# Kernel optimization log

Measured on AMD Instinct MI355X. Metric: run time of the kernel, lower is better.

## Reference

```python
import jax, jax.numpy as jnp
import numpy as np


def _pairwise_dist(x):
    # Euclidean (p=2) pairwise distances via Gram identity; avoids the
    # [N, N, D] broadcasted difference tensor the torch code materializes.
    sq = jnp.sum(x * x, axis=1)                      # [N]
    d2 = sq[:, None] + sq[None, :] - 2.0 * (x @ x.T)  # [N, N]
    return jnp.sqrt(jnp.clip(d2, 0.0))


def _persistence_pairs(dist_np):
    """0-dim persistent homology pairs = MST edges via Kruskal union-find,
    processed in order of increasing edge weight (matches the repo's
    PersistentHomologyCalculation). Returns [N-1, 2] int64 index pairs."""
    n = dist_np.shape[0]
    iu, ju = np.triu_indices(n, k=1)
    order = np.argsort(dist_np[iu, ju], kind='stable')
    parent = np.arange(n)

    def find(i):
        root = i
        while parent[root] != root:
            root = parent[root]
        while parent[i] != root:  # path compression
            parent[i], i = root, parent[i]
        return root

    pairs = []
    for e in order:
        a, b = find(iu[e]), find(ju[e])
        if a != b:
            parent[a] = b
            pairs.append((iu[e], ju[e]))
            if len(pairs) == n - 1:
                break
    return np.asarray(pairs, dtype=np.int64)


def setup_inputs() -> dict:
    key = jax.random.key(0)
    x = jax.random.normal(key, (2048, 4096), dtype=jnp.float32)
    return {"x": x}


def reference(x):
    distances = _pairwise_dist(x)  # [N, N]
    # Pair selection is done on host on detached values, as in the original
    # (pairs have fixed count N-1, so the output shape is static).
    pairs = _persistence_pairs(np.asarray(jax.device_get(distances)))
    i = jnp.asarray(pairs[:, 0])
    j = jnp.asarray(pairs[:, 1])
    selected_distances = distances[i, j]  # [N-1]
    return selected_distances
```

## Files before the change

kernel.cpp:

```cpp
#include <hip/hip_runtime.h>
#include <stdint.h>

#define NPTS 2048
#define KDIM 4096
#define INVALID_KEY 0xFFFFFFFFFFFFFFFFull

typedef __bf16 bf16x8 __attribute__((ext_vector_type(8)));
typedef float f32x4 __attribute__((ext_vector_type(4)));

__device__ __forceinline__ unsigned short f2bf(float f) {
    unsigned int u = __float_as_uint(f);
    u = (u + 0x7FFFu + ((u >> 16) & 1u)) >> 16;
    return (unsigned short)u;
}

__device__ __forceinline__ void gld_lds16(const unsigned short* g, unsigned short* l) {
    __builtin_amdgcn_global_load_lds(
        (const __attribute__((address_space(1))) unsigned int*)g,
        (__attribute__((address_space(3))) unsigned int*)l, 16, 0, 0);
}

__device__ __forceinline__ unsigned long long mk_key(float w, int i, int j) {
    unsigned long long a = (i < j) ? i : j;
    unsigned long long b = (i < j) ? j : i;
    return ((unsigned long long)__float_as_uint(w) << 22) | (a << 11) | b;
}

__global__ __launch_bounds__(256) void convert_sqnorm_kernel(const float* __restrict__ x,
                                                             unsigned short* __restrict__ xb,
                                                             float* __restrict__ sq,
                                                             int* __restrict__ comp0,
                                                             unsigned long long* __restrict__ best0,
                                                             int* __restrict__ ctl) {
    const int row = blockIdx.x;
    const float* xr = x + (size_t)row * KDIM;
    unsigned short* xbr = xb + (size_t)row * KDIM;
    const int t = threadIdx.x;
    float s = 0.f;
    #pragma unroll
    for (int k = 0; k < 4; ++k) {
        int c = t * 4 + k * 1024;
        float4 v = *(const float4*)(xr + c);
        s += v.x * v.x + v.y * v.y + v.z * v.z + v.w * v.w;
        uint2 u;
        u.x = (unsigned)f2bf(v.x) | ((unsigned)f2bf(v.y) << 16);
        u.y = (unsigned)f2bf(v.z) | ((unsigned)f2bf(v.w) << 16);
        *(uint2*)(xbr + c) = u;
    }
    for (int off = 32; off; off >>= 1) s += __shfl_down(s, off);
    __shared__ float p[4];
    if ((t & 63) == 0) p[t >> 6] = s;
    __syncthreads();
    if (t == 0) {
        sq[row] = p[0] + p[1] + p[2] + p[3];
        comp0[row] = row;
        best0[row] = INVALID_KEY;
        if (row == 0) { ctl[0] = 0; ctl[1] = 0; }
    }
}

__global__ __launch_bounds__(256, 2) void gemm_d2_glds(const unsigned short* __restrict__ xb,
                                                       const float* __restrict__ sq,
                                                       float* __restrict__ D2,
                                                       unsigned long long* __restrict__ best0) {
    __shared__ __align__(16) unsigned short tile[12 * 512];
    const int I0 = blockIdx.y * 64;
    const int J0 = blockIdx.x * 128;
    const int t = threadIdx.x;
    const int lane = t & 63;
    const int w = t >> 6;
    const int m = lane & 15, q = lane >> 4;

    const int rp = lane >> 2;
    const int sg = (lane & 3) ^ ((lane >> 3) & 3);
    const unsigned short* gsrc[3]; unsigned short* ldst[3];
    #pragma unroll
    for (int ci = 0; ci < 3; ++ci) {
        int c = w * 3 + ci;
        int rowbase = (c < 4) ? (I0 + c * 16) : (J0 + (c - 4) * 16);
        gsrc[ci] = xb + (size_t)(rowbase + rp) * KDIM + sg * 8;
        ldst[ci] = tile + c * 512;
    }
    const int fro = m * 32 + ((q ^ ((m >> 1) & 3)) * 8);

    f32x4 acc[4][2] = {};
    for (int kc = 0; kc < KDIM; kc += 32) {
        #pragma unroll
        for (int ci = 0; ci < 3; ++ci) gld_lds16(gsrc[ci] + kc, ldst[ci]);
        __syncthreads();
        bf16x8 af[4], bg[2];
        #pragma unroll
        for (int rt = 0; rt < 4; ++rt)
            af[rt] = *(const bf16x8*)(tile + rt * 512 + fro);
        #pragma unroll
        for (int ct = 0; ct < 2; ++ct)
            bg[ct] = *(const bf16x8*)(tile + (4 + w * 2 + ct) * 512 + fro);
        #pragma unroll
        for (int rt = 0; rt < 4; ++rt)
            #pragma unroll
            for (int ct = 0; ct < 2; ++ct)
                acc[rt][ct] = __builtin_amdgcn_mfma_f32_16x16x32_bf16(
                    af[rt], bg[ct], acc[rt][ct], 0, 0, 0);
        __syncthreads();
    }

    unsigned long long* s_best = (unsigned long long*)tile;
    if (t < 64) s_best[t] = INVALID_KEY;
    __syncthreads();
    #pragma unroll
    for (int rt = 0; rt < 4; ++rt) {
        #pragma unroll
        for (int r = 0; r < 4; ++r) {
            int i = I0 + rt * 16 + q * 4 + r;
            unsigned long long kk = INVALID_KEY;
            #pragma unroll
            for (int ct = 0; ct < 2; ++ct) {
                int j = J0 + w * 32 + ct * 16 + m;
                float v = sq[i] + sq[j] - 2.0f * acc[rt][ct][r];
                v = (i == j) ? __builtin_inff() : fmaxf(v, 0.0f);
                D2[(size_t)i * NPTS + j] = v;
                if (i != j) {
                    unsigned long long key = mk_key(v, i, j);
                    kk = (key < kk) ? key : kk;
                }
            }
            #pragma unroll
            for (int mask = 1; mask < 16; mask <<= 1) {
                unsigned long long o = __shfl_xor(kk, mask);
                kk = (o < kk) ? o : kk;
            }
            if (m == 0) atomicMin(&s_best[rt * 16 + q * 4 + r], kk);
        }
    }
    __syncthreads();
    if (t < 64) atomicMin(&best0[I0 + t], s_best[t]);
}

__global__ __launch_bounds__(256) void boruvka_round(const float* __restrict__ D2,
                                                     const unsigned long long* __restrict__ bestP,
                                                     unsigned long long* __restrict__ bestN,
                                                     const int* __restrict__ compP,
                                                     int* __restrict__ compN,
                                                     float* __restrict__ ew,
                                                     int* __restrict__ ctl) {
    if (ctl[1]) return;
    __shared__ int sc[NPTS];
    __shared__ unsigned long long compBest[NPTS];
    __shared__ int par[NPTS];
    __shared__ int s_wsum[4];
    __shared__ int s_nroots;
    const int t = threadIdx.x;
    const int bid = blockIdx.x;
    const int lane = t & 63, w = t >> 6;

    if (t == 0) s_nroots = 0;
    #pragma unroll
    for (int e = 0; e < 8; ++e) {
        int v = t * 8 + e;
        sc[v] = compP[v];
        compBest[v] = INVALID_KEY;
    }
    __syncthreads();

    unsigned long long kreg[8]; int oreg[8];
    #pragma unroll
    for (int e = 0; e < 8; ++e) {
        int v = t * 8 + e;
        unsigned long long k = bestP[v];
        kreg[e] = k;
        int a = (int)((k >> 11) & 2047), b = (int)(k & 2047);
        oreg[e] = (a == v) ? b : a;
        if (k != INVALID_KEY && sc[oreg[e]] != sc[v])
            atomicMin(&compBest[sc[v]], k);
    }
    __syncthreads();

    bool isr[8];
    #pragma unroll
    for (int e = 0; e < 8; ++e) {
        int c = t * 8 + e;
        int p = c;
        isr[e] = (sc[c] == c);
        if (isr[e]) {
            unsigned long long k = compBest[c];
            if (k != INVALID_KEY) {
                int a = (int)((k >> 11) & 2047), b = (int)(k & 2047);
                int j = (sc[a] == c) ? b : a;
                int rj = sc[j];
                bool mutual = (compBest[rj] == k);
                if (!(mutual && c < rj)) {
                    p = rj;
                    if (bid == 0)
                        ew[atomicAdd(&ctl[0], 1)] = __uint_as_float((unsigned)(k >> 22));
                }
            }
        }
        par[c] = p;
    }
    int any = __syncthreads_or(1);
    do {
        int local = 0;
        #pragma unroll
        for (int e = 0; e < 8; ++e) {
            if (isr[e]) {
                int c = t * 8 + e;
                int p = par[c];
                int np = par[p];
                if (np != p) { par[c] = np; local = 1; }
            }
        }
        any = __syncthreads_or(local);
    } while (any);

    int newsc[8]; int rc = 0;
    #pragma unroll
    for (int e = 0; e < 8; ++e) {
        int v = t * 8 + e;
        newsc[e] = par[sc[v]];
        if (newsc[e] == v) rc++;
    }
    if (rc) atomicAdd(&s_nroots, rc);
    __syncthreads();
    #pragma unroll
    for (int e = 0; e < 8; ++e) sc[t * 8 + e] = newsc[e];
    __syncthreads();
    const int nroots = s_nroots;

    if (bid == 0) {
        #pragma unroll
        for (int e = 0; e < 8; ++e) compN[t * 8 + e] = newsc[e];
        if (t == 0 && nroots == 1) ctl[1] = 1;
    }
    if (nroots == 1) return;

    int flags[8], lc = 0;
    #pragma unroll
    for (int e = 0; e < 8; ++e) {
        int v = t * 8 + e;
        flags[e] = (kreg[e] == INVALID_KEY) || (sc[oreg[e]] == sc[v]);
        lc += flags[e];
    }
    int scn = lc;
    #pragma unroll
    for (int d = 1; d < 64; d <<= 1) {
        int o = __shfl_up(scn, d);
        if (lane >= d) scn += o;
    }
    if (lane == 63) s_wsum[w] = scn;
    __syncthreads();
    int wbase = 0;
    for (int i = 0; i < w; ++i) wbase += s_wsum[i];
    const int cnt = s_wsum[0] + s_wsum[1] + s_wsum[2] + s_wsum[3];
    int base = wbase + scn - lc;
    int* rlist = par;
    #pragma unroll
    for (int e = 0; e < 8; ++e)
        if (flags[e]) rlist[base++] = t * 8 + e;
    __syncthreads();

    if (t < 4) {
        int v = bid * 4 + t;
        unsigned long long k = bestP[v];
        if (k != INVALID_KEY) {
            int a = (int)((k >> 11) & 2047), b = (int)(k & 2047);
            int o = (a == v) ? b : a;
            if (sc[o] != sc[v]) bestN[v] = k;
        }
    }
    int widx = bid * 4 + w;
    if (widx < cnt) {
        int v = rlist[widx];
        int mc = sc[v];
        const float* row = D2 + (size_t)v * NPTS;
        unsigned long long best = INVALID_KEY;
        #pragma unroll
        for (int k = 0; k < 8; ++k) {
            int j0 = k * 256 + lane * 4;
            float4 w4 = *(const float4*)(row + j0);
            int4 c4 = *(const int4*)(sc + j0);
            float wa[4] = {w4.x, w4.y, w4.z, w4.w};
            int ca[4] = {c4.x, c4.y, c4.z, c4.w};
            #pragma unroll
            for (int e = 0; e < 4; ++e) {
                if (ca[e] != mc) {
                    unsigned long long key = mk_key(wa[e], v, j0 + e);
                    best = (key < best) ? key : best;
                }
            }
        }
        for (int off = 32; off; off >>= 1) {
            unsigned long long o = __shfl_down(best, off);
            best = (o < best) ? o : best;
        }
        if (lane == 0) bestN[v] = best;
    }
}

__global__ __launch_bounds__(1024) void sort_out_kernel(const float* __restrict__ ew,
                                                        float* __restrict__ out) {
    __shared__ float wl[NPTS];
    const int t = threadIdx.x;
    for (int i = t; i < NPTS; i += 1024)
        wl[i] = (i < NPTS - 1) ? ew[i] : __builtin_inff();
    __syncthreads();
    for (int k = 2; k <= NPTS; k <<= 1) {
        for (int j = k >> 1; j > 0; j >>= 1) {
            for (int i = t; i < NPTS; i += 1024) {
                int l = i ^ j;
                if (l > i) {
                    float a = wl[i], b = wl[l];
                    bool up = ((i & k) == 0);
                    if ((a > b) == up) { wl[i] = b; wl[l] = a; }
                }
            }
            __syncthreads();
        }
    }
    for (int i = t; i < NPTS - 1; i += 1024)
        out[i] = sqrtf(fmaxf(wl[i], 0.0f));
}

extern "C" void kernel_launch(void* const* d_in, const int* in_sizes, int n_in,
                              void* d_out, int out_size, void* d_ws, size_t ws_size,
                              hipStream_t stream) {
    const float* x = (const float*)d_in[0];
    float* out = (float*)d_out;
    char* ws = (char*)d_ws;
    unsigned short* xb = (unsigned short*)ws;
    float* D2 = (float*)(ws + 16777216);
    size_t o = 33554432;
    float* sq = (float*)(ws + o);                  o += 8192;
    unsigned long long* best0 = (unsigned long long*)(ws + o); o += 16384;
    unsigned long long* best1 = (unsigned long long*)(ws + o); o += 16384;
    int* comp0 = (int*)(ws + o);                   o += 8192;
    int* comp1 = (int*)(ws + o);                   o += 8192;
    float* ew = (float*)(ws + o);                  o += 8192;
    int* ctl = (int*)(ws + o);

    hipLaunchKernelGGL(convert_sqnorm_kernel, dim3(NPTS), dim3(256), 0, stream,
                       x, xb, sq, comp0, best0, ctl);
    hipLaunchKernelGGL(gemm_d2_glds, dim3(16, 32), dim3(256), 0, stream,
                       xb, sq, D2, best0);
    for (int r = 0; r < 11; ++r) {
        unsigned long long* bp = (r & 1) ? best1 : best0;
        unsigned long long* bn = (r & 1) ? best0 : best1;
        int* cp = (r & 1) ? comp1 : comp0;
        int* cn = (r & 1) ? comp0 : comp1;
        hipLaunchKernelGGL(boruvka_round, dim3(512), dim3(256), 0, stream,
                           D2, bp, bn, cp, cn, ew, ctl);
    }
    hipLaunchKernelGGL(sort_out_kernel, dim3(1), dim3(1024), 0, stream, ew, out);
}
```

Before: 229.0 us.

## Remap GEMM blocks per XCD, split 64-bit LDS atomics, drop one Boruvka round

The GEMM launch becomes a 1D grid, and block ids are remapped so that tiles sharing rows and columns land on the same XCD, which should improve L2 reuse. In the Boruvka round, the per-component 64-bit LDS atomicMin is replaced by two 32-bit passes: a min over the weight first, then a min over the edge id among the tied weights, at the cost of an extra barrier. The round count drops from 11 to 10. That skips a kernel launch but risks leaving the MST incomplete if 10 rounds are ever not enough.

```diff
diff --git a/kernel.cpp b/kernel.cpp
--- a/kernel.cpp
+++ b/kernel.cpp
@@ -64,8 +64,12 @@
                                                        float* __restrict__ D2,
                                                        unsigned long long* __restrict__ best0) {
     __shared__ __align__(16) unsigned short tile[12 * 512];
-    const int I0 = blockIdx.y * 64;
-    const int J0 = blockIdx.x * 128;
+    const int id = blockIdx.x;
+    const int xcd = id & 7, u0 = id >> 3;
+    const int by = (xcd & 3) * 8 + (u0 & 7);
+    const int bx = (xcd >> 2) * 8 + (u0 >> 3);
+    const int I0 = by * 64;
+    const int J0 = bx * 128;
     const int t = threadIdx.x;
     const int lane = t & 63;
     const int w = t >> 6;
@@ -145,7 +149,8 @@
                                                      int* __restrict__ ctl) {
     if (ctl[1]) return;
     __shared__ int sc[NPTS];
-    __shared__ unsigned long long compBest[NPTS];
+    __shared__ unsigned compW[NPTS];
+    __shared__ unsigned compI[NPTS];
     __shared__ int par[NPTS];
     __shared__ int s_wsum[4];
     __shared__ int s_nroots;
@@ -158,21 +163,29 @@
     for (int e = 0; e < 8; ++e) {
         int v = t * 8 + e;
         sc[v] = compP[v];
-        compBest[v] = INVALID_KEY;
-    }
-    __syncthreads();
-
-    unsigned long long kreg[8]; int oreg[8];
+        compW[v] = 0xFFFFFFFFu;
+        compI[v] = 0xFFFFFFFFu;
+    }
+    __syncthreads();
+
+    unsigned long long kreg[8]; int oreg[8], scv[8]; unsigned w32[8], id22[8]; bool ext[8];
     #pragma unroll
     for (int e = 0; e < 8; ++e) {
         int v = t * 8 + e;
         unsigned long long k = bestP[v];
         kreg[e] = k;
-        int a = (int)((k >> 11) & 2047), b = (int)(k & 2047);
+        w32[e] = (unsigned)(k >> 22);
+        id22[e] = (unsigned)(k & 0x3FFFFFu);
+        int a = (int)((id22[e] >> 11) & 2047), b = (int)(id22[e] & 2047);
         oreg[e] = (a == v) ? b : a;
-        if (k != INVALID_KEY && sc[oreg[e]] != sc[v])
-            atomicMin(&compBest[sc[v]], k);
-    }
+        scv[e] = sc[v];
+        ext[e] = (k != INVALID_KEY) && (sc[oreg[e]] != scv[e]);
+        if (ext[e]) atomicMin(&compW[scv[e]], w32[e]);
+    }
+    __syncthreads();
+    #pragma unroll
+    for (int e = 0; e < 8; ++e)
+        if (ext[e] && w32[e] == compW[scv[e]]) atomicMin(&compI[scv[e]], id22[e]);
     __syncthreads();
 
     bool isr[8];
@@ -182,16 +195,17 @@
         int p = c;
         isr[e] = (sc[c] == c);
         if (isr[e]) {
-            unsigned long long k = compBest[c];
-            if (k != INVALID_KEY) {
-                int a = (int)((k >> 11) & 2047), b = (int)(k & 2047);
+            unsigned wv = compW[c];
+            if (wv != 0xFFFFFFFFu) {
+                unsigned id = compI[c];
+                int a = (int)((id >> 11) & 2047), b = (int)(id & 2047);
                 int j = (sc[a] == c) ? b : a;
                 int rj = sc[j];
-                bool mutual = (compBest[rj] == k);
+                bool mutual = (compW[rj] == wv) && (compI[rj] == id);
                 if (!(mutual && c < rj)) {
                     p = rj;
                     if (bid == 0)
-                        ew[atomicAdd(&ctl[0], 1)] = __uint_as_float((unsigned)(k >> 22));
+                        ew[atomicAdd(&ctl[0], 1)] = __uint_as_float(wv);
                 }
             }
         }
@@ -262,7 +276,8 @@
         int v = bid * 4 + t;
         unsigned long long k = bestP[v];
         if (k != INVALID_KEY) {
-            int a = (int)((k >> 11) & 2047), b = (int)(k & 2047);
+            unsigned id = (unsigned)(k & 0x3FFFFFu);
+            int a = (int)((id >> 11) & 2047), b = (int)(id & 2047);
             int o = (a == v) ? b : a;
             if (sc[o] != sc[v]) bestN[v] = k;
         }
@@ -339,9 +354,9 @@
 
     hipLaunchKernelGGL(convert_sqnorm_kernel, dim3(NPTS), dim3(256), 0, stream,
                        x, xb, sq, comp0, best0, ctl);
-    hipLaunchKernelGGL(gemm_d2_glds, dim3(16, 32), dim3(256), 0, stream,
+    hipLaunchKernelGGL(gemm_d2_glds, dim3(512), dim3(256), 0, stream,
                        xb, sq, D2, best0);
-    for (int r = 0; r < 11; ++r) {
+    for (int r = 0; r < 10; ++r) {
         unsigned long long* bp = (r & 1) ? best1 : best0;
         unsigned long long* bn = (r & 1) ? best0 : best1;
         int* cp = (r & 1) ? comp1 : comp0;
```

After: 236.4 us. 1.03x slower.
